# Optimization experiments

Hardware: AMD Instinct MI355X
Metric: run time of the kernel (lower is better)

The kernel has to match this reference:

```python
import jax, jax.numpy as jnp
from jax import lax
import numpy as np

B, T, F = 32, 8192, 16
HID = 128
OUT = 24
K1 = 10


def setup_inputs() -> dict:
    key = jax.random.key(0)
    ks = jax.random.split(key, 5)
    x = jax.random.normal(ks[0], (B, T, F), dtype=jnp.float32)
    # Conv1d(F -> HID, kernel=10): weight (O, I, K), bias (O,)
    w1 = jax.random.normal(ks[1], (HID, F, K1), dtype=jnp.float32) * (1.0 / np.sqrt(F * K1))
    b1 = jax.random.normal(ks[2], (HID,), dtype=jnp.float32) * 0.01
    # Linear(HID*10 -> OUT): weight (OUT, HID*10), bias (OUT,)
    wf = jax.random.normal(ks[3], (OUT, HID * K1), dtype=jnp.float32) * (1.0 / np.sqrt(HID * K1))
    bf = jax.random.normal(ks[4], (OUT,), dtype=jnp.float32) * 0.01
    return {"x": x, "w1": w1, "b1": b1, "wf": wf, "bf": bf}


def reference(x, w1, b1, wf, bf):
    # x: (B, T, F) -> (B, F, T)
    xc = jnp.transpose(x, (0, 2, 1))
    # Conv1d k=10, pad=9 -> length T+9
    h = lax.conv_general_dilated(
        xc, w1, window_strides=(1,), padding=[(9, 9)],
        dimension_numbers=("NCH", "OIH", "NCH")) + b1[None, :, None]  # (B, HID, T+9)
    # out[:, :x.shape[2], :] keeps the first T timesteps
    h = h[:, :, :x.shape[1]]
    h = jnp.concatenate([jnp.repeat(h[:, :, :1], 9, axis=2), h], axis=2)
    # Per-step Linear over flattened 10-step windows == valid conv with k=10.
    # flatten order of window (10, C) is time-major: col index = t*C + c
    kf = jnp.transpose(wf.reshape(wf.shape[0], K1, -1), (0, 2, 1))  # (OUT, HID, 10)
    y = lax.conv_general_dilated(
        h, kf, window_strides=(1,), padding="VALID",
        dimension_numbers=("NCH", "OIH", "NCH")) + bf[None, :, None]  # (B, OUT, T)
    return jnp.transpose(y, (0, 2, 1))  # (B, T, OUT)
```

## Files before the change

kernel.cpp:

```cpp
#include <hip/hip_runtime.h>

#define B_   32
#define T_   8192
#define F_   16
#define OUT_ 24
#define K1_  10
#define ND   19
#define JP   32
#define TB   512
#define WROWS 536
#define H1OFF (WROWS * 8 + 8)

#define WS_BC_OFF   20480
#define WS_E_OFF    20576
#define WS_W1T_OFF  144992

typedef short short8 __attribute__((ext_vector_type(8)));
typedef float float4v __attribute__((ext_vector_type(4)));

__device__ __forceinline__ unsigned short f2bf(float f) {
    unsigned u = __builtin_bit_cast(unsigned, f);
    unsigned r = (u + 0x7fffu + ((u >> 16) & 1u)) >> 16;
    return (unsigned short)r;
}

__device__ __forceinline__ short8 cvt8(float4 f0, float4 f1) {
    short8 v;
    v[0] = (short)f2bf(f0.x); v[1] = (short)f2bf(f0.y);
    v[2] = (short)f2bf(f0.z); v[3] = (short)f2bf(f0.w);
    v[4] = (short)f2bf(f1.x); v[5] = (short)f2bf(f1.y);
    v[6] = (short)f2bf(f1.z); v[7] = (short)f2bf(f1.w);
    return v;
}

__global__ __launch_bounds__(256) void pre_kernel(const float* __restrict__ w1,
                                                  float* __restrict__ w1t,
                                                  unsigned short* __restrict__ w2pk) {
    int bx = blockIdx.x;
    int tid = threadIdx.x;
    if (bx < 80) {
        int idx = bx * 256 + tid;
        float v = w1[idx];
        int c = idx / 160;
        int rem = idx - c * 160;
        int i = rem / 10;
        int k = rem - i * 10;
        w1t[(k * 16 + i) * 128 + c] = v;
    } else {
        int idx = (bx - 80) * 256 + tid;
        ((unsigned*)w2pk)[idx] = 0;
    }
}

__global__ __launch_bounds__(256) void prep_kernel(const float* __restrict__ w1t,
                                                   const float* __restrict__ b1,
                                                   const float* __restrict__ wf,
                                                   const float* __restrict__ bf,
                                                   unsigned short* __restrict__ w2pk,
                                                   float* __restrict__ bcg,
                                                   float* __restrict__ Eg) {
    int tid = threadIdx.x;
    int lane = tid & 63;
    int wid = blockIdx.x * 4 + (tid >> 6);

    if (wid < 456) {
        int j = wid / ND, d = wid % ND;
        float p[16];
#pragma unroll
        for (int i = 0; i < 16; ++i) p[i] = 0.f;
        int klo = d - 9 > 0 ? d - 9 : 0;
        int khi = d < 9 ? d : 9;
        for (int k = klo; k <= khi; ++k) {
            float w0 = wf[j * 1280 + k * 128 + lane];
            float w1v = wf[j * 1280 + k * 128 + 64 + lane];
            const float* wb = w1t + (d - k) * 16 * 128;
#pragma unroll
            for (int i = 0; i < 16; ++i)
                p[i] = fmaf(w0, wb[i * 128 + lane], fmaf(w1v, wb[i * 128 + 64 + lane], p[i]));
        }
#pragma unroll
        for (int i = 0; i < 16; ++i) {
            p[i] += __shfl_xor(p[i], 1);
            p[i] += __shfl_xor(p[i], 2);
            p[i] += __shfl_xor(p[i], 4);
            p[i] += __shfl_xor(p[i], 8);
            p[i] += __shfl_xor(p[i], 16);
            p[i] += __shfl_xor(p[i], 32);
        }
        if (lane < 16) {
            float v = p[0];
#pragma unroll
            for (int i = 1; i < 16; ++i)
                if (lane == i) v = p[i];
            int kk = d * 16 + lane;
            int ks = kk >> 5, r = kk & 31;
            int quad = r >> 3, z = r & 7;
            int tbl = j >> 4, jj = j & 15;
            int lt = jj + quad * 16;
            w2pk[((tbl * 10 + ks) * 64 + lt) * 8 + z] = f2bf(v);
        }
    } else if (wid < 480) {
        int j = wid - 456;
        float s0 = 0.f, s1 = 0.f;
#pragma unroll
        for (int k = 0; k < K1_; ++k) {
            s0 += wf[j * 1280 + k * 128 + lane];
            s1 += wf[j * 1280 + k * 128 + 64 + lane];
        }
        float s = s0 * b1[lane] + s1 * b1[64 + lane];
        s += __shfl_xor(s, 1);
        s += __shfl_xor(s, 2);
        s += __shfl_xor(s, 4);
        s += __shfl_xor(s, 8);
        s += __shfl_xor(s, 16);
        s += __shfl_xor(s, 32);
        if (lane == 0) bcg[j] = bf[j] + s;
    } else {
        int eidx = wid - 480;
        int t = eidx / 216;
        int rem = eidx % 216;
        int j = rem / 9, tau = rem % 9;
        float p[16];
#pragma unroll
        for (int i = 0; i < 16; ++i) p[i] = 0.f;
        for (int k = 0; k < K1_; ++k) {
            int u = t + k - 9; if (u < 0) u = 0;
            if (tau > u) continue;
            int kap = tau + 9 - u;
            float w0 = wf[j * 1280 + k * 128 + lane];
            float w1v = wf[j * 1280 + k * 128 + 64 + lane];
            const float* wb = w1t + kap * 16 * 128;
#pragma unroll
            for (int i = 0; i < 16; ++i)
                p[i] = fmaf(w0, wb[i * 128 + lane], fmaf(w1v, wb[i * 128 + 64 + lane], p[i]));
        }
#pragma unroll
        for (int i = 0; i < 16; ++i) {
            p[i] += __shfl_xor(p[i], 1);
            p[i] += __shfl_xor(p[i], 2);
            p[i] += __shfl_xor(p[i], 4);
            p[i] += __shfl_xor(p[i], 8);
            p[i] += __shfl_xor(p[i], 16);
            p[i] += __shfl_xor(p[i], 32);
        }
        if (lane < 16) {
            float v = p[0];
#pragma unroll
            for (int i = 1; i < 16; ++i)
                if (lane == i) v = p[i];
            Eg[((t * OUT_ + j) * 9 + tau) * 16 + lane] = v;
        }
    }
}

__global__ __launch_bounds__(256) void main_kernel(const float* __restrict__ x,
                                                   const unsigned short* __restrict__ w2pk,
                                                   const float* __restrict__ bcg,
                                                   float* __restrict__ out,
                                                   const float* __restrict__ Eg) {
    int tid = threadIdx.x;
    int b = blockIdx.y;

    if (blockIdx.x == 16) {
        if (tid >= 9 * OUT_) return;
        int t = tid / OUT_, j = tid % OUT_;
        const float4* xv = (const float4*)(x + (long)b * T_ * F_);
        const float4* ev = (const float4*)(Eg + (long)tid * 144);
        float ax = 0.f, ay = 0.f, az = 0.f, aw = 0.f;
#pragma unroll
        for (int q = 0; q < 36; ++q) {
            float4 e = ev[q];
            float4 v = xv[q];
            ax = fmaf(e.x, v.x, ax);
            ay = fmaf(e.y, v.y, ay);
            az = fmaf(e.z, v.z, az);
            aw = fmaf(e.w, v.w, aw);
        }
        out[((long)b * T_ + t) * OUT_ + j] = bcg[j] + ((ax + ay) + (az + aw));
        return;
    }

    __shared__ short xls[2 * WROWS * 8 + 8];
    int t0 = blockIdx.x * TB;

    for (int idx = tid; idx < 2 * WROWS; idx += 256) {
        int h = idx >= WROWS;
        int row = h ? idx - WROWS : idx;
        int t = t0 - 18 + row;
        short8 v = short8{0, 0, 0, 0, 0, 0, 0, 0};
        if (t >= 0 && t < T_) {
            const float4* p = (const float4*)(x + ((long)b * T_ + t) * 16 + h * 8);
            v = cvt8(p[0], p[1]);
        }
        *(short8*)(xls + h * H1OFF + row * 8) = v;
    }

    int lane = tid & 63, w = tid >> 6;
    int t = lane & 15, q = lane >> 4;
    int h = q & 1, qh = q >> 1;

    const unsigned short* pk0 = w2pk + lane * 8;
    const unsigned short* pk1 = w2pk + 5120 + lane * 8;
    short8 W0[10], W1[10];
#pragma unroll
    for (int ks = 0; ks < 10; ++ks) {
        W0[ks] = *(const short8*)(pk0 + ks * 512);
        W1[ks] = *(const short8*)(pk1 + ks * 512);
    }

    __syncthreads();

    const short* ap = xls + h * H1OFF + (w * 128 + t + qh) * 8;

    float4v acc[8][2];
#pragma unroll
    for (int mt = 0; mt < 8; ++mt) {
        acc[mt][0] = float4v{0.f, 0.f, 0.f, 0.f};
        acc[mt][1] = float4v{0.f, 0.f, 0.f, 0.f};
    }

#pragma unroll
    for (int ks = 0; ks < 10; ++ks) {
#pragma unroll
        for (int mt = 0; mt < 8; ++mt) {
            short8 xf = *(const short8*)(ap + (mt * 16 + 2 * ks) * 8);
            acc[mt][0] = __builtin_amdgcn_mfma_f32_16x16x32_bf16(W0[ks], xf, acc[mt][0], 0, 0, 0);
            acc[mt][1] = __builtin_amdgcn_mfma_f32_16x16x32_bf16(W1[ks], xf, acc[mt][1], 0, 0, 0);
        }
    }

    long outb = (long)b * T_;
    float4 bc0 = *(const float4*)(bcg + q * 4);
    float4 bc1 = (q < 2) ? *(const float4*)(bcg + 16 + q * 4) : make_float4(0.f, 0.f, 0.f, 0.f);
    bool edge = (blockIdx.x == 0);
#pragma unroll
    for (int mt = 0; mt < 8; ++mt) {
        int t_out = t0 + w * 128 + mt * 16 + t;
        if (!edge || t_out >= 9) {
            float* o = out + (outb + t_out) * OUT_;
            float4 v0 = make_float4(acc[mt][0][0] + bc0.x, acc[mt][0][1] + bc0.y,
                                    acc[mt][0][2] + bc0.z, acc[mt][0][3] + bc0.w);
            *(float4*)(o + q * 4) = v0;
            if (q < 2) {
                float4 v1 = make_float4(acc[mt][1][0] + bc1.x, acc[mt][1][1] + bc1.y,
                                        acc[mt][1][2] + bc1.z, acc[mt][1][3] + bc1.w);
                *(float4*)(o + 16 + q * 4) = v1;
            }
        }
    }
}

extern "C" void kernel_launch(void* const* d_in, const int* in_sizes, int n_in,
                              void* d_out, int out_size, void* d_ws, size_t ws_size,
                              hipStream_t stream) {
    const float* x  = (const float*)d_in[0];
    const float* w1 = (const float*)d_in[1];
    const float* b1 = (const float*)d_in[2];
    const float* wf = (const float*)d_in[3];
    const float* bf = (const float*)d_in[4];
    float* out = (float*)d_out;
    unsigned short* w2pk = (unsigned short*)d_ws;
    float* bcg = (float*)((char*)d_ws + WS_BC_OFF);
    float* Eg  = (float*)((char*)d_ws + WS_E_OFF);
    float* w1t = (float*)((char*)d_ws + WS_W1T_OFF);

    hipLaunchKernelGGL(pre_kernel, dim3(120), dim3(256), 0, stream, w1, w1t, w2pk);
    hipLaunchKernelGGL(prep_kernel, dim3(606), dim3(256), 0, stream,
                       w1t, b1, wf, bf, w2pk, bcg, Eg);
    hipLaunchKernelGGL(main_kernel, dim3(17, B_), dim3(256), 0, stream,
                       x, w2pk, bcg, out, Eg);
}
```

Baseline: 98.17 us.

## Fuse weight prep into one kernel and compute boundary rows directly from conv

Merges the transpose pre-kernel into the weight-folding prep kernel. Each block now stages w1 in swizzled shared memory and builds the transposed copy there, which removes one launch. The precomputed edge-effect tensor E is dropped. The first nine output rows are instead computed in the main kernel's extra block by evaluating the hidden conv for the first timesteps and then the linear layer. This cuts prep work and launch count, but every prep block now reloads all of w1, and the boundary block does more serial work.

```diff
diff --git a/kernel.cpp b/kernel.cpp
--- a/kernel.cpp
+++ b/kernel.cpp
@@ -6,14 +6,12 @@
 #define OUT_ 24
 #define K1_  10
 #define ND   19
-#define JP   32
 #define TB   512
 #define WROWS 536
 #define H1OFF (WROWS * 8 + 8)
 
 #define WS_BC_OFF   20480
-#define WS_E_OFF    20576
-#define WS_W1T_OFF  144992
+#define WS_W1T_OFF  20576
 
 typedef short short8 __attribute__((ext_vector_type(8)));
 typedef float float4v __attribute__((ext_vector_type(4)));
@@ -33,51 +31,72 @@
     return v;
 }
 
-__global__ __launch_bounds__(256) void pre_kernel(const float* __restrict__ w1,
-                                                  float* __restrict__ w1t,
-                                                  unsigned short* __restrict__ w2pk) {
-    int bx = blockIdx.x;
-    int tid = threadIdx.x;
-    if (bx < 80) {
-        int idx = bx * 256 + tid;
-        float v = w1[idx];
-        int c = idx / 160;
-        int rem = idx - c * 160;
-        int i = rem / 10;
-        int k = rem - i * 10;
-        w1t[(k * 16 + i) * 128 + c] = v;
-    } else {
-        int idx = (bx - 80) * 256 + tid;
-        ((unsigned*)w2pk)[idx] = 0;
-    }
-}
-
-__global__ __launch_bounds__(256) void prep_kernel(const float* __restrict__ w1t,
+__global__ __launch_bounds__(256) void prep_kernel(const float* __restrict__ w1,
                                                    const float* __restrict__ b1,
                                                    const float* __restrict__ wf,
                                                    const float* __restrict__ bf,
                                                    unsigned short* __restrict__ w2pk,
                                                    float* __restrict__ bcg,
-                                                   float* __restrict__ Eg) {
+                                                   float* __restrict__ w1t) {
     int tid = threadIdx.x;
+    int bx = blockIdx.x;
     int lane = tid & 63;
-    int wid = blockIdx.x * 4 + (tid >> 6);
-
-    if (wid < 456) {
-        int j = wid / ND, d = wid % ND;
-        float p[16];
-#pragma unroll
-        for (int i = 0; i < 16; ++i) p[i] = 0.f;
+
+    if (bx < 160) {
+        __shared__ float wl[160 * 64];
+        int wid = bx * 4 + (tid >> 6);
+        int j = wid / 20;
+        int d = wid - j * 20;
+        bool active = (j < 24) && (d < 19);
         int klo = d - 9 > 0 ? d - 9 : 0;
         int khi = d < 9 ? d : 9;
-        for (int k = klo; k <= khi; ++k) {
-            float w0 = wf[j * 1280 + k * 128 + lane];
-            float w1v = wf[j * 1280 + k * 128 + 64 + lane];
-            const float* wb = w1t + (d - k) * 16 * 128;
-#pragma unroll
-            for (int i = 0; i < 16; ++i)
-                p[i] = fmaf(w0, wb[i * 128 + lane], fmaf(w1v, wb[i * 128 + 64 + lane], p[i]));
-        }
+
+        float p[16];
+#pragma unroll
+        for (int i = 0; i < 16; ++i) p[i] = 0.f;
+
+        const float4* w4 = (const float4*)w1;
+        for (int half = 0; half < 2; ++half) {
+            for (int n = 0; n < 10; ++n) {
+                int f4 = half * 2560 + n * 256 + tid;
+                float4 v = w4[f4];
+                int f = f4 * 4;
+#pragma unroll
+                for (int m = 0; m < 4; ++m) {
+                    int ff = f + m;
+                    int c = ff / 160;
+                    int rem = ff - c * 160;
+                    int i = rem / 10;
+                    int k = rem - i * 10;
+                    int row = k * 16 + i;
+                    int cc = c - half * 64;
+                    float e = (m == 0) ? v.x : (m == 1) ? v.y : (m == 2) ? v.z : v.w;
+                    wl[row * 64 + (cc ^ (row & 31))] = e;
+                }
+            }
+            __syncthreads();
+
+            if (active) {
+                for (int k = klo; k <= khi; ++k) {
+                    float wv = wf[j * 1280 + k * 128 + half * 64 + lane];
+                    int rb = (d - k) * 16;
+#pragma unroll
+                    for (int i = 0; i < 16; ++i) {
+                        int row = rb + i;
+                        p[i] = fmaf(wv, wl[row * 64 + (lane ^ (row & 31))], p[i]);
+                    }
+                }
+            }
+            if (bx == 0) {
+                for (int n = 0; n < 40; ++n) {
+                    int idx = n * 256 + tid;
+                    int row = idx >> 6, cc = idx & 63;
+                    w1t[row * 128 + half * 64 + cc] = wl[row * 64 + (cc ^ (row & 31))];
+                }
+            }
+            if (half == 0) __syncthreads();
+        }
+
 #pragma unroll
         for (int i = 0; i < 16; ++i) {
             p[i] += __shfl_xor(p[i], 1);
@@ -99,8 +118,8 @@
             int lt = jj + quad * 16;
             w2pk[((tbl * 10 + ks) * 64 + lt) * 8 + z] = f2bf(v);
         }
-    } else if (wid < 480) {
-        int j = wid - 456;
+    } else {
+        int j = (bx - 160) * 4 + (tid >> 6);
         float s0 = 0.f, s1 = 0.f;
 #pragma unroll
         for (int k = 0; k < K1_; ++k) {
@@ -115,41 +134,6 @@
         s += __shfl_xor(s, 16);
         s += __shfl_xor(s, 32);
         if (lane == 0) bcg[j] = bf[j] + s;
-    } else {
-        int eidx = wid - 480;
-        int t = eidx / 216;
-        int rem = eidx % 216;
-        int j = rem / 9, tau = rem % 9;
-        float p[16];
-#pragma unroll
-        for (int i = 0; i < 16; ++i) p[i] = 0.f;
-        for (int k = 0; k < K1_; ++k) {
-            int u = t + k - 9; if (u < 0) u = 0;
-            if (tau > u) continue;
-            int kap = tau + 9 - u;
-            float w0 = wf[j * 1280 + k * 128 + lane];
-            float w1v = wf[j * 1280 + k * 128 + 64 + lane];
-            const float* wb = w1t + kap * 16 * 128;
-#pragma unroll
-            for (int i = 0; i < 16; ++i)
-                p[i] = fmaf(w0, wb[i * 128 + lane], fmaf(w1v, wb[i * 128 + 64 + lane], p[i]));
-        }
-#pragma unroll
-        for (int i = 0; i < 16; ++i) {
-            p[i] += __shfl_xor(p[i], 1);
-            p[i] += __shfl_xor(p[i], 2);
-            p[i] += __shfl_xor(p[i], 4);
-            p[i] += __shfl_xor(p[i], 8);
-            p[i] += __shfl_xor(p[i], 16);
-            p[i] += __shfl_xor(p[i], 32);
-        }
-        if (lane < 16) {
-            float v = p[0];
-#pragma unroll
-            for (int i = 1; i < 16; ++i)
-                if (lane == i) v = p[i];
-            Eg[((t * OUT_ + j) * 9 + tau) * 16 + lane] = v;
-        }
     }
 }
 
@@ -157,30 +141,63 @@
                                                    const unsigned short* __restrict__ w2pk,
                                                    const float* __restrict__ bcg,
                                                    float* __restrict__ out,
-                                                   const float* __restrict__ Eg) {
+                                                   const float* __restrict__ w1t,
+                                                   const float* __restrict__ wf,
+                                                   const float* __restrict__ b1,
+                                                   const float* __restrict__ bf) {
     int tid = threadIdx.x;
     int b = blockIdx.y;
+    __shared__ __align__(16) short xls[2 * WROWS * 8 + 8];
 
     if (blockIdx.x == 16) {
-        if (tid >= 9 * OUT_) return;
-        int t = tid / OUT_, j = tid % OUT_;
-        const float4* xv = (const float4*)(x + (long)b * T_ * F_);
-        const float4* ev = (const float4*)(Eg + (long)tid * 144);
-        float ax = 0.f, ay = 0.f, az = 0.f, aw = 0.f;
-#pragma unroll
-        for (int q = 0; q < 36; ++q) {
-            float4 e = ev[q];
-            float4 v = xv[q];
-            ax = fmaf(e.x, v.x, ax);
-            ay = fmaf(e.y, v.y, ay);
-            az = fmaf(e.z, v.z, az);
-            aw = fmaf(e.w, v.w, aw);
-        }
-        out[((long)b * T_ + t) * OUT_ + j] = bcg[j] + ((ax + ay) + (az + aw));
+        float* xh   = (float*)xls;
+        float* hbuf = xh + 304;
+
+        for (int idx = tid; idx < 304; idx += 256) {
+            int m = idx >> 4, i = idx & 15;
+            int tr = m - 9;
+            xh[idx] = (tr >= 0) ? x[((long)b * T_ + tr) * 16 + i] : 0.f;
+        }
+        __syncthreads();
+
+        int c = tid & 127, uh = tid >> 7;
+        float hacc[5];
+        float bv = b1[c];
+#pragma unroll
+        for (int uu = 0; uu < 5; ++uu) hacc[uu] = bv;
+        const float* xu = xh + (uh * 5) * 16;
+        for (int r = 0; r < 160; ++r) {
+            float wv = w1t[r * 128 + c];
+#pragma unroll
+            for (int uu = 0; uu < 5; ++uu)
+                hacc[uu] = fmaf(wv, xu[uu * 16 + r], hacc[uu]);
+        }
+#pragma unroll
+        for (int uu = 0; uu < 5; ++uu) hbuf[(uh * 5 + uu) * 132 + c] = hacc[uu];
+        __syncthreads();
+
+        if (tid < 9 * OUT_) {
+            int t = tid / OUT_, j = tid - (tid / OUT_) * OUT_;
+            float ax = 0.f, ay = 0.f, az = 0.f, aw = 0.f;
+            for (int k = 0; k < K1_; ++k) {
+                int m = t + k - 9; if (m < 0) m = 0;
+                const float4* hv = (const float4*)(hbuf + m * 132);
+                const float4* wv = (const float4*)(wf + j * 1280 + k * 128);
+#pragma unroll
+                for (int q = 0; q < 32; ++q) {
+                    float4 h4 = hv[q];
+                    float4 w4 = wv[q];
+                    ax = fmaf(w4.x, h4.x, ax);
+                    ay = fmaf(w4.y, h4.y, ay);
+                    az = fmaf(w4.z, h4.z, az);
+                    aw = fmaf(w4.w, h4.w, aw);
+                }
+            }
+            out[((long)b * T_ + t) * OUT_ + j] = bf[j] + ((ax + ay) + (az + aw));
+        }
         return;
     }
 
-    __shared__ short xls[2 * WROWS * 8 + 8];
     int t0 = blockIdx.x * TB;
 
     for (int idx = tid; idx < 2 * WROWS; idx += 256) {
@@ -261,12 +278,10 @@
     float* out = (float*)d_out;
     unsigned short* w2pk = (unsigned short*)d_ws;
     float* bcg = (float*)((char*)d_ws + WS_BC_OFF);
-    float* Eg  = (float*)((char*)d_ws + WS_E_OFF);
     float* w1t = (float*)((char*)d_ws + WS_W1T_OFF);
 
-    hipLaunchKernelGGL(pre_kernel, dim3(120), dim3(256), 0, stream, w1, w1t, w2pk);
-    hipLaunchKernelGGL(prep_kernel, dim3(606), dim3(256), 0, stream,
-                       w1t, b1, wf, bf, w2pk, bcg, Eg);
+    hipLaunchKernelGGL(prep_kernel, dim3(166), dim3(256), 0, stream,
+                       w1, b1, wf, bf, w2pk, bcg, w1t);
     hipLaunchKernelGGL(main_kernel, dim3(17, B_), dim3(256), 0, stream,
-                       x, w2pk, bcg, out, Eg);
-}
+                       x, w2pk, bcg, out, w1t, wf, b1, bf);
+}
```

After: 131.3 us. 33.7% more time.
